# Kernel tuning notes

Measured on AMD Instinct MI355X. Metric: run time of the kernel, lower is better.

The kernel has to match this reference:

```python
import jax, jax.numpy as jnp
import numpy as np
from jax import lax

TOP_K = 200
IOU_THR = 0.5
SCORE_FLOOR = 0.01  # torch code breaks when top score < 0.01

BATCH, N_ANCHOR, N_CLASS_FG = 32, 24564, 80  # last dim of x = 4 + 1 + 80 = 85


def setup_inputs() -> dict:
    key = jax.random.key(0)
    k1, k2 = jax.random.split(key)
    x = jax.random.normal(k1, (BATCH, N_ANCHOR, 4 + 1 + N_CLASS_FG), dtype=jnp.float32)
    # anchors: (cx, cy, w, h) in normalized coords
    anchor = jax.random.uniform(k2, (N_ANCHOR, 4), dtype=jnp.float32, minval=0.05, maxval=0.95)
    return {"x": x, "anchor": anchor}


def _iou_one_vs_all(box1, boxes):
    # box1: [4] (x1,y1,x2,y2); boxes: [N,4] -> ious [N]
    b1x1, b1y1, b1x2, b1y2 = box1[0], box1[1], box1[2], box1[3]
    b2x1, b2y1, b2x2, b2y2 = boxes[:, 0], boxes[:, 1], boxes[:, 2], boxes[:, 3]
    area1 = (b1x2 - b1x1) * (b1y2 - b1y1)
    area2 = (b2x2 - b2x1) * (b2y2 - b2y1)
    xl = jnp.maximum(b1x1, b2x1)
    xr = jnp.minimum(b1x2, b2x2)
    yt = jnp.maximum(b1y1, b2y1)
    yb = jnp.minimum(b1y2, b2y2)
    # torch code clamps intersection extents to [0, 1]
    common = jnp.clip(xr - xl, 0.0, 1.0) * jnp.clip(yb - yt, 0.0, 1.0)
    return common / (area1 + area2 - common)


def _nms_single(cls_i, score_i, box_i):
    # cls_i [N] int, score_i [N], box_i [N,4] -> keep [TOP_K, 6]
    order = jnp.argsort(-score_i)  # descending
    c = cls_i[order].astype(box_i.dtype)
    s = score_i[order]
    b = box_i[order]
    dets = jnp.concatenate([c[:, None], s[:, None], b], axis=1)  # [N, 6]
    valid0 = jnp.ones((dets.shape[0],), dtype=bool)

    def step(valid, _):
        idx = jnp.argmax(valid)  # first still-valid (highest-score) box
        ok = valid[idx] & (s[idx] >= SCORE_FLOOR)
        row = jnp.where(ok, dets[idx], jnp.zeros((6,), dets.dtype))
        ious = _iou_one_vs_all(b[idx], b)  # [N]
        new_valid = valid & (ious < IOU_THR)
        new_valid = new_valid.at[idx].set(False)
        valid = jnp.where(ok, new_valid, valid)
        return valid, row

    _, keep = lax.scan(step, valid0, None, length=TOP_K)
    return keep  # [TOP_K, 6] = (class, score, x1, y1, x2, y2)


def _postprocess(x, anchor):
    # decode boxes
    d = x[:, :, :4]                          # [B, A, 4]
    ax, ay, aw, ah = (anchor[None, :, i] for i in range(4))  # each [1, A]
    cx = d[:, :, 0] * aw / 10.0 + ax
    cy = d[:, :, 1] * ah / 10.0 + ay
    w = jnp.exp(d[:, :, 2] / 5.0) * aw
    h = jnp.exp(d[:, :, 3] / 5.0) * ah
    box = jnp.stack([cx - w / 2.0, cy - h / 2.0, cx + w / 2.0, cy + h / 2.0], axis=2)  # [B,A,4] x1y1x2y2
    # class scores: softmax over (bg + fg), then max over foreground classes
    probs = jax.nn.softmax(x[:, :, 4:], axis=2)
    fg = probs[:, :, 1:]
    score = jnp.max(fg, axis=2)              # [B, A]
    cls = jnp.argmax(fg, axis=2)             # [B, A] foreground class index
    return jax.vmap(_nms_single)(cls, score, box)  # [B, TOP_K, 6]


def reference(x, anchor):
    return _postprocess(x, anchor)
```

## Files before the change

### kernel.cpp

```cpp
#include <hip/hip_runtime.h>
#include <math.h>

#define NB   32
#define NA   24564
#define NTOT (NB * NA)
#define NCH  85
#define TOPK 200
#define IOU_THR_F     0.5f
#define SCORE_FLOOR_F 0.01f

#define DEC_T 128

#define NMS_T 512
#define NSUB  8
#define GTH   (NSUB * NMS_T)
#define SL    6
#define KP    16
#define NLOC  17
#define NPOOL (2 * NMS_T)
#define CKADDR(e) ((((e) & 15) << 6) | ((e) >> 4))

#define ENT_SZ      32
#define LIST_SZ     (16 + NLOC * ENT_SZ)
#define BATCH_LISTS (NSUB * LIST_SZ)
#define LISTS_BUF   (NB * BATCH_LISTS)

__global__ __launch_bounds__(DEC_T) void decode_kernel(
    const float* __restrict__ x, const float* __restrict__ anchor,
    float4* __restrict__ boxes, float* __restrict__ scores,
    float* __restrict__ clsf, unsigned* __restrict__ arrive)
{
    __shared__ float tile[DEC_T * NCH];

    if (blockIdx.x == 0 && threadIdx.x < NB) arrive[threadIdx.x] = 0u;

    const int base = blockIdx.x * DEC_T;
    const float4* src = (const float4*)(x + (size_t)base * NCH);
    float4* dst = (float4*)tile;
    for (int k = threadIdx.x; k < DEC_T * NCH / 4; k += DEC_T) dst[k] = src[k];
    __syncthreads();

    const int g = base + threadIdx.x;
    const int i = g % NA;
    const float* row = tile + threadIdx.x * NCH;

    float ax = anchor[i * 4 + 0];
    float ay = anchor[i * 4 + 1];
    float aw = anchor[i * 4 + 2];
    float ah = anchor[i * 4 + 3];

    float d0 = row[0], d1 = row[1], d2 = row[2], d3 = row[3];
    float cx = __fadd_rn(__fdiv_rn(__fmul_rn(d0, aw), 10.0f), ax);
    float cy = __fadd_rn(__fdiv_rn(__fmul_rn(d1, ah), 10.0f), ay);
    float w = __fmul_rn((float)exp((double)__fdiv_rn(d2, 5.0f)), aw);
    float h = __fmul_rn((float)exp((double)__fdiv_rn(d3, 5.0f)), ah);
    float hw = __fmul_rn(w, 0.5f);
    float hh = __fmul_rn(h, 0.5f);
    boxes[g] = make_float4(__fsub_rn(cx, hw), __fsub_rn(cy, hh),
                           __fadd_rn(cx, hw), __fadd_rn(cy, hh));

    const float* z = row + 4;
    float m = z[0];
    #pragma unroll 9
    for (int k = 1; k < 81; k++) m = fmaxf(m, z[k]);

    double S = 0.0;
    double be = 0.0;
    float  bz = -INFINITY;
    int    bj = 0;
    for (int k = 0; k < 81; k++) {
        float zk = z[k];
        double e = exp((double)__fsub_rn(zk, m));
        S += e;
        if (k >= 1 && zk > bz) { bz = zk; be = e; bj = k - 1; }
    }
    scores[g] = (float)(be / S);
    clsf[g]   = (float)bj;
}

__device__ __forceinline__ bool suppressed_by(const float4 v, const float a2,
                                              const float4 w, const float a1)
{
    float xl = fmaxf(w.x, v.x);
    float xr = fminf(w.z, v.z);
    float yt = fmaxf(w.y, v.y);
    float yb = fminf(w.w, v.w);
    float cw  = fminf(fmaxf(__fsub_rn(xr, xl), 0.0f), 1.0f);
    float chh = fminf(fmaxf(__fsub_rn(yb, yt), 0.0f), 1.0f);
    float common = __fmul_rn(cw, chh);
    float denom  = __fsub_rn(__fadd_rn(a1, a2), common);
    float iou    = __fdiv_rn(common, denom);
    return !(iou < IOU_THR_F);
}

__device__ __forceinline__ unsigned wave_umax_dpp(unsigned v)
{
    int x = (int)v;
    #define DPP_ST(C) { \
        int y_ = __builtin_amdgcn_update_dpp(x, x, C, 0xF, 0xF, false); \
        x = ((unsigned)y_ > (unsigned)x) ? y_ : x; }
    DPP_ST(0x111) DPP_ST(0x112) DPP_ST(0x114) DPP_ST(0x118)
    DPP_ST(0x142) DPP_ST(0x143)
    #undef DPP_ST
    return (unsigned)__builtin_amdgcn_readlane(x, 63);
}

__global__ __launch_bounds__(NMS_T, 1) void nms_kernel(
    const float4* __restrict__ boxes, const float* __restrict__ scores,
    const float* __restrict__ clsf, float* __restrict__ out,
    char* __restrict__ lists, unsigned* __restrict__ arrive)
{
    __shared__ unsigned s_cs[NPOOL];
    __shared__ unsigned s_cl[NPOOL];
    __shared__ float4   s_cbox[NPOOL];
    __shared__ float4   s_stage4[BATCH_LISTS / 16];

    const int b    = blockIdx.x >> 3;
    const int sub  = blockIdx.x & 7;
    const int tid  = threadIdx.x;
    const int lane = tid & 63;
    const int gtid = sub * NMS_T + tid;
    const float*  sc = scores + (size_t)b * NA;
    const float4* bx = boxes  + (size_t)b * NA;
    const float*  cf = clsf   + (size_t)b * NA;
    float* ob = out + (size_t)b * TOPK * 6;
    unsigned* arr = arrive + b;

    float4 box[SL]; float a2[SL]; unsigned long long skey[SL];
    unsigned am = 0;
    #pragma unroll
    for (int s = 0; s < SL; s++) {
        int j = gtid + s * GTH;
        box[s] = make_float4(0.f, 0.f, 0.f, 0.f); a2[s] = 0.f; skey[s] = 0ULL;
        if (j < NA) {
            box[s] = bx[j];
            a2[s]  = __fmul_rn(__fsub_rn(box[s].z, box[s].x),
                               __fsub_rn(box[s].w, box[s].y));
            skey[s] = ((unsigned long long)__float_as_uint(sc[j]) << 32) |
                      ((unsigned long long)(unsigned)(NA - j) << 10);
            am |= 1u << s;
        }
    }

    unsigned long long wr0 = 0ULL, wr1 = 0ULL;
    int np_prev = 0;
    int t = 0; bool gdone = false; int pass = 0;

    while (true) {
        if (np_prev > 0) {
            for (int k = 0; k < np_prev; k++) {
                unsigned byte = (unsigned)(((k < 8) ? (wr0 >> (8 * k))
                                                    : (wr1 >> (8 * (k - 8)))) & 0xFF);
                int wl = byte >> 5, wi = byte & 31;
                const unsigned* hdr = (const unsigned*)s_stage4 + wl * (LIST_SZ / 4);
                const unsigned* eb  = hdr + 4 + wi * (ENT_SZ / 4);
                unsigned long long wkey = *(const unsigned long long*)eb;
                float  wa = *(const float*)(eb + 2);
                float4 wb = *(const float4*)(eb + 4);
                int jw = NA - (int)((wkey >> 10) & 0x7FFFULL);
                if ((jw & (GTH - 1)) == gtid) am &= ~(1u << (jw >> 12));
                #pragma unroll
                for (int s = 0; s < SL; s++)
                    if (am & (1u << s))
                        if (suppressed_by(box[s], a2[s], wb, wa)) am &= ~(1u << s);
            }
        }

        {
            unsigned long long k1 = 0ULL, k2 = 0ULL; int s1 = -1, s2 = -1;
            #pragma unroll
            for (int s = 0; s < SL; s++) {
                if (!(am & (1u << s))) continue;
                unsigned long long kk = skey[s];
                if (kk > k1)      { k2 = k1; s2 = s1; k1 = kk; s1 = s; }
                else if (kk > k2) { k2 = kk; s2 = s; }
            }
            int e0 = 2 * tid, e1 = 2 * tid + 1;
            s_cs[CKADDR(e0)] = (s1 >= 0) ? (unsigned)(k1 >> 32) : 1u;
            s_cl[CKADDR(e0)] = (unsigned)k1 | (unsigned)e0;
            s_cs[CKADDR(e1)] = (s2 >= 0) ? (unsigned)(k2 >> 32) : 1u;
            s_cl[CKADDR(e1)] = (unsigned)k2 | (unsigned)e1;
            if (s1 >= 0) s_cbox[e0] = bx[gtid + s1 * GTH];
            if (s2 >= 0) s_cbox[e1] = bx[gtid + s2 * GTH];
        }
        __syncthreads();

        char* Lb = lists + (size_t)(pass & 1) * LISTS_BUF
                         + (size_t)b * BATCH_LISTS + (size_t)sub * LIST_SZ;
        {
            unsigned cs[16], cl[16];
            #pragma unroll
            for (int i = 0; i < 16; i++) {
                cs[i] = s_cs[(i << 6) | lane];
                cl[i] = s_cl[(i << 6) | lane];
            }
            int cnt = 0; unsigned long long hb = 0ULL, lastk = 0ULL, bound = 0ULL;
            while (true) {
                unsigned msl = 0u;
                #pragma unroll
                for (int i = 0; i < 16; i++) msl = (cs[i] > msl) ? cs[i] : msl;
                unsigned ms = wave_umax_dpp(msl);
                unsigned lol = 0u;
                #pragma unroll
                for (int i = 0; i < 16; i++)
                    if (cs[i] == ms) lol = (cl[i] > lol) ? cl[i] : lol;
                unsigned lo = wave_umax_dpp(lol);
                unsigned long long lm = ((unsigned long long)ms << 32) | lo;

                if (!(lm > hb)) { bound = hb; break; }
                if (!(__uint_as_float(ms) >= SCORE_FLOOR_F)) { bound = 0ULL; break; }

                int e = (int)(lo & 1023u);
                float4 cb = s_cbox[e];
                float  ca = __fmul_rn(__fsub_rn(cb.z, cb.x), __fsub_rn(cb.w, cb.y));
                if (tid == 0) {
                    char* ep = Lb + 16 + cnt * ENT_SZ;
                    *(unsigned long long*)ep = lm;
                    *(float*)(ep + 8)        = ca;
                    *(float4*)(ep + 16)      = cb;
                }
                lastk = lm;
                int olane = e >> 4, oi = e & 15;
                unsigned pks = 0u;
                #pragma unroll
                for (int i = 0; i < 16; i++) if (i == (oi ^ 1)) pks = cs[i];
                unsigned pkol = (unsigned)__builtin_amdgcn_readlane((int)pks, olane);
                if (pkol == 0u) hb = lm;
                bool me = (lane == olane);
                #pragma unroll
                for (int i = 0; i < 16; i++) if (i == oi && me) cs[i] = 0u;
                cnt++;
                if (cnt == NLOC) { bound = lastk; break; }
            }
            if (tid == 0) {
                *(unsigned*)Lb = (unsigned)cnt;
                *(unsigned long long*)(Lb + 8) = bound;
            }
        }
        __threadfence();
        __syncthreads();

        if (tid == 0) {
            __hip_atomic_fetch_add(arr, 1u, __ATOMIC_ACQ_REL,
                                   __HIP_MEMORY_SCOPE_AGENT);
            unsigned tgt = (unsigned)(NSUB * (pass + 1));
            while (__hip_atomic_load(arr, __ATOMIC_ACQUIRE,
                                     __HIP_MEMORY_SCOPE_AGENT) < tgt)
                __builtin_amdgcn_s_sleep(2);
        }
        __syncthreads();

        {
            const unsigned* g = (const unsigned*)(lists
                + (size_t)(pass & 1) * LISTS_BUF + (size_t)b * BATCH_LISTS);
            unsigned* dst = (unsigned*)s_stage4;
            for (int i = tid; i < BATCH_LISTS / 4; i += NMS_T)
                dst[i] = __hip_atomic_load(g + i, __ATOMIC_ACQUIRE,
                                           __HIP_MEMORY_SCOPE_AGENT);
        }
        __syncthreads();

        unsigned long long cur64 = 0ULL;
        unsigned long long exb = 0ULL;
        unsigned long long nwr0 = 0ULL, nwr1 = 0ULL;
        int np = 0;
        int kmaxp = TOPK - t; if (kmaxp > KP) kmaxp = KP;
        #pragma unroll
        for (int lb2 = 0; lb2 < NSUB; lb2++) {
            const unsigned* hdr = (const unsigned*)s_stage4 + lb2 * (LIST_SZ / 4);
            if (hdr[0] == 0u) {
                unsigned long long bo = *(const unsigned long long*)(hdr + 2);
                if (bo > exb) exb = bo;
            }
        }
        while (true) {
            unsigned long long best = 0ULL; int bl = -1;
            #pragma unroll
            for (int lb2 = 0; lb2 < NSUB; lb2++) {
                const unsigned* hdr = (const unsigned*)s_stage4 + lb2 * (LIST_SZ / 4);
                unsigned c = (unsigned)((cur64 >> (8 * lb2)) & 0xFF);
                if (c < hdr[0]) {
                    unsigned long long k =
                        *(const unsigned long long*)(hdr + 4 + c * (ENT_SZ / 4));
                    if (k > best) { best = k; bl = lb2; }
                }
            }
            if (!(best > exb)) { if (best == 0ULL && exb == 0ULL) gdone = true; break; }
            float bscore = __uint_as_float((unsigned)(best >> 32));
            if (!(bscore >= SCORE_FLOOR_F)) { gdone = true; break; }

            unsigned ci = (unsigned)((cur64 >> (8 * bl)) & 0xFF);
            const unsigned* hdr = (const unsigned*)s_stage4 + bl * (LIST_SZ / 4);
            const unsigned* eb  = hdr + 4 + ci * (ENT_SZ / 4);
            float  ca2 = *(const float*)(eb + 2);
            float4 cb2 = *(const float4*)(eb + 4);

            bool kill = false;
            for (int k = 0; k < np; k++) {
                unsigned byte = (unsigned)(((k < 8) ? (nwr0 >> (8 * k))
                                                    : (nwr1 >> (8 * (k - 8)))) & 0xFF);
                int wl = byte >> 5, wi = byte & 31;
                const unsigned* wh = (const unsigned*)s_stage4 + wl * (LIST_SZ / 4);
                const unsigned* we = wh + 4 + wi * (ENT_SZ / 4);
                float  wa = *(const float*)(we + 2);
                float4 wb = *(const float4*)(we + 4);
                kill |= suppressed_by(cb2, ca2, wb, wa);
            }
            cur64 += (1ULL << (8 * bl));
            if (((cur64 >> (8 * bl)) & 0xFF) == hdr[0]) {
                unsigned long long bo = *(const unsigned long long*)(hdr + 2);
                if (bo > exb) exb = bo;
            }
            if (!kill) {
                unsigned byte = (unsigned)((bl << 5) | (int)ci);
                if (np < 8) nwr0 |= ((unsigned long long)byte) << (8 * np);
                else        nwr1 |= ((unsigned long long)byte) << (8 * (np - 8));
                int jw = NA - (int)((best >> 10) & 0x7FFFULL);
                if ((jw & (GTH - 1)) == gtid) {
                    float* o6 = ob + (size_t)(t + np) * 6;
                    o6[0] = cf[jw]; o6[1] = bscore;
                    o6[2] = cb2.x; o6[3] = cb2.y; o6[4] = cb2.z; o6[5] = cb2.w;
                }
                np++;
                if (np == kmaxp) break;
            }
        }
        wr0 = nwr0; wr1 = nwr1; np_prev = np;
        t += np; pass++;
        if (gdone || t >= TOPK) break;
    }

    if (sub == 0)
        for (int k = t * 6 + tid; k < TOPK * 6; k += NMS_T) ob[k] = 0.0f;
}

extern "C" void kernel_launch(void* const* d_in, const int* in_sizes, int n_in,
                              void* d_out, int out_size, void* d_ws, size_t ws_size,
                              hipStream_t stream) {
    const float* x      = (const float*)d_in[0];
    const float* anchor = (const float*)d_in[1];
    float* out = (float*)d_out;

    char* ws = (char*)d_ws;
    const size_t boxes_bytes  = (size_t)NTOT * 16;
    const size_t scores_off   = (boxes_bytes + 255) & ~255ULL;
    const size_t scores_bytes = (size_t)NTOT * 4;
    const size_t cls_off      = (scores_off + scores_bytes + 255) & ~255ULL;
    const size_t lists_off    = (cls_off + scores_bytes + 255) & ~255ULL;
    const size_t arrive_off   = (lists_off + 2 * (size_t)LISTS_BUF + 255) & ~255ULL;

    float4*   boxes  = (float4*)ws;
    float*    scores = (float*)(ws + scores_off);
    float*    clsf   = (float*)(ws + cls_off);
    char*     lists  = ws + lists_off;
    unsigned* arrive = (unsigned*)(ws + arrive_off);

    decode_kernel<<<NTOT / DEC_T, DEC_T, 0, stream>>>(x, anchor, boxes, scores,
                                                      clsf, arrive);
    nms_kernel<<<NB * NSUB, NMS_T, 0, stream>>>(boxes, scores, clsf, out,
                                                lists, arrive);
}
```

Before: 1.953 ms.

## Double NMS winners per pass and cache winner boxes in shared arrays

```diff
diff --git a/kernel.cpp b/kernel.cpp
--- a/kernel.cpp
+++ b/kernel.cpp
@@ -15,8 +15,8 @@
 #define NSUB  8
 #define GTH   (NSUB * NMS_T)
 #define SL    6
-#define KP    16
-#define NLOC  17
+#define KP    32
+#define NLOC  32
 #define NPOOL (2 * NMS_T)
 #define CKADDR(e) ((((e) & 15) << 6) | ((e) >> 4))
 
@@ -114,6 +114,9 @@
     __shared__ unsigned s_cl[NPOOL];
     __shared__ float4   s_cbox[NPOOL];
     __shared__ float4   s_stage4[BATCH_LISTS / 16];
+    __shared__ float4   s_wbox[KP];
+    __shared__ float    s_warea[KP];
+    __shared__ int      s_wj[KP];
 
     const int b    = blockIdx.x >> 3;
     const int sub  = blockIdx.x & 7;
@@ -142,28 +145,19 @@
         }
     }
 
-    unsigned long long wr0 = 0ULL, wr1 = 0ULL;
     int np_prev = 0;
     int t = 0; bool gdone = false; int pass = 0;
 
     while (true) {
-        if (np_prev > 0) {
-            for (int k = 0; k < np_prev; k++) {
-                unsigned byte = (unsigned)(((k < 8) ? (wr0 >> (8 * k))
-                                                    : (wr1 >> (8 * (k - 8)))) & 0xFF);
-                int wl = byte >> 5, wi = byte & 31;
-                const unsigned* hdr = (const unsigned*)s_stage4 + wl * (LIST_SZ / 4);
-                const unsigned* eb  = hdr + 4 + wi * (ENT_SZ / 4);
-                unsigned long long wkey = *(const unsigned long long*)eb;
-                float  wa = *(const float*)(eb + 2);
-                float4 wb = *(const float4*)(eb + 4);
-                int jw = NA - (int)((wkey >> 10) & 0x7FFFULL);
-                if ((jw & (GTH - 1)) == gtid) am &= ~(1u << (jw >> 12));
-                #pragma unroll
-                for (int s = 0; s < SL; s++)
-                    if (am & (1u << s))
-                        if (suppressed_by(box[s], a2[s], wb, wa)) am &= ~(1u << s);
-            }
+        for (int k = 0; k < np_prev; k++) {
+            float4 wb = s_wbox[k];
+            float  wa = s_warea[k];
+            int    jw = s_wj[k];
+            if ((jw & (GTH - 1)) == gtid) am &= ~(1u << (jw >> 12));
+            #pragma unroll
+            for (int s = 0; s < SL; s++)
+                if (am & (1u << s))
+                    if (suppressed_by(box[s], a2[s], wb, wa)) am &= ~(1u << s);
         }
 
         {
@@ -262,7 +256,6 @@
 
         unsigned long long cur64 = 0ULL;
         unsigned long long exb = 0ULL;
-        unsigned long long nwr0 = 0ULL, nwr1 = 0ULL;
         int np = 0;
         int kmaxp = TOPK - t; if (kmaxp > KP) kmaxp = KP;
         #pragma unroll
@@ -296,26 +289,21 @@
             float4 cb2 = *(const float4*)(eb + 4);
 
             bool kill = false;
-            for (int k = 0; k < np; k++) {
-                unsigned byte = (unsigned)(((k < 8) ? (nwr0 >> (8 * k))
-                                                    : (nwr1 >> (8 * (k - 8)))) & 0xFF);
-                int wl = byte >> 5, wi = byte & 31;
-                const unsigned* wh = (const unsigned*)s_stage4 + wl * (LIST_SZ / 4);
-                const unsigned* we = wh + 4 + wi * (ENT_SZ / 4);
-                float  wa = *(const float*)(we + 2);
-                float4 wb = *(const float4*)(we + 4);
-                kill |= suppressed_by(cb2, ca2, wb, wa);
-            }
+            for (int k = 0; k < np; k++)
+                kill |= suppressed_by(cb2, ca2, s_wbox[k], s_warea[k]);
+
             cur64 += (1ULL << (8 * bl));
             if (((cur64 >> (8 * bl)) & 0xFF) == hdr[0]) {
                 unsigned long long bo = *(const unsigned long long*)(hdr + 2);
                 if (bo > exb) exb = bo;
             }
             if (!kill) {
-                unsigned byte = (unsigned)((bl << 5) | (int)ci);
-                if (np < 8) nwr0 |= ((unsigned long long)byte) << (8 * np);
-                else        nwr1 |= ((unsigned long long)byte) << (8 * (np - 8));
                 int jw = NA - (int)((best >> 10) & 0x7FFFULL);
+                if (lane == 0) {
+                    s_wbox[np]  = cb2;
+                    s_warea[np] = ca2;
+                    s_wj[np]    = jw;
+                }
                 if ((jw & (GTH - 1)) == gtid) {
                     float* o6 = ob + (size_t)(t + np) * 6;
                     o6[0] = cf[jw]; o6[1] = bscore;
@@ -325,7 +313,7 @@
                 if (np == kmaxp) break;
             }
         }
-        wr0 = nwr0; wr1 = nwr1; np_prev = np;
+        np_prev = np;
         t += np; pass++;
         if (gdone || t >= TOPK) break;
     }
```

New measurement: 1.801 ms. 7.8% less time.
